# Kernel tuning notes

Hardware: AMD Instinct MI355X
Metric: run time of the kernel (lower is better)

Reference implementation:

```python
import jax, jax.numpy as jnp
import numpy as np

E, L, M, F, S, P = 4, 10, 512, 128, 1000, 10  # envs, labels, max_sample, features, sample_size, batch_len


def setup_inputs() -> dict:
    key = jax.random.key(0)
    k1, k2, k3 = jax.random.split(key, 3)
    data_len = jax.random.randint(k1, (E, L), M // 2, M + 1, dtype=jnp.int32)
    matrix = jax.random.normal(k2, (E, L, M, F), dtype=jnp.float32)
    # zero out padded samples beyond data_len (as shape_to_matrix does)
    pad_mask = jnp.arange(M)[None, None, :, None] < data_len[:, :, None, None]
    matrix = matrix * pad_mask
    params = jnp.eye(F, dtype=jnp.float32) + 0.01 * jax.random.normal(k3, (F, F), dtype=jnp.float32)
    is_train_env = jnp.array([True, True, False, False])
    return {"matrix": matrix, "params": params, "data_len": data_len, "is_train_env": is_train_env}


def reference(matrix, params, data_len, is_train_env):
    lenf = data_len.astype(matrix.dtype)  # [E,L], torch keeps this as float32
    # __init__ preprocessing: normalize by mean std over sample dim (detached in torch)
    std = jax.lax.stop_gradient(jnp.std(matrix, axis=2).mean())
    mat = matrix / std
    # Silverman-style bandwidth on the normalized matrix (detached in torch)
    bw = jax.lax.stop_gradient(1.06 * (M ** (-1.0 / 5.0)) * jnp.std(mat, axis=2).mean())
    offset = jnp.exp(-0.5 / bw ** 2)
    proj = jnp.einsum('elmf,fg->elmg', mat, params)  # [E,L,M,F]
    left = jax.lax.stop_gradient(proj.min())   # .item() in torch -> constant
    right = jax.lax.stop_gradient(proj.max())
    delta = (right - left) / S
    x_grid = jnp.linspace(left, right, S)
    divisor = jnp.sqrt(2.0 * jnp.pi) * bw

    def step(acc, points):  # points: [P] grid chunk
        d2 = (proj[..., None] - points) ** 2                     # [E,L,M,F,P]
        s = jnp.sum(offset ** d2, axis=2)                        # [E,L,F,P]
        # remove contribution of zero-padded samples, then normalize by true count
        corr = (M - lenf)[:, :, None] * (offset ** (points ** 2))[None, None, :]  # [E,L,P]
        r = (s - corr[:, :, None, :]) / lenf[:, :, None, None]   # [E,L,F,P]
        d = jnp.sum(jnp.abs(r[:, None] - r[None, :]), axis=-1)   # [E,E,L,F] pairwise L1 over grid chunk
        return acc + d, None

    store_dis, _ = jax.lax.scan(step, jnp.zeros((E, E, L, F), proj.dtype), x_grid.reshape(S // P, P))
    store_dis = store_dis / divisor  # [E,E,L,F]

    idx = jnp.arange(E)
    upper = idx[:, None] < idx[None, :]                                   # all env pairs i<j
    train_pair = upper & is_train_env[:, None] & is_train_env[None, :]    # train env pairs i<j
    half = store_dis * (delta / 2.0)
    neg = jnp.array(-jnp.inf, half.dtype)
    test_results = jnp.where(upper[:, :, None, None], half, neg).max(axis=(0, 1))        # [L,F]
    train_results = jnp.where(train_pair[:, :, None, None], half, neg).max(axis=(0, 1))  # [L,F]
    train_dis = train_results.max(axis=0).mean()
    test_dis = test_results.max(axis=0).mean()
    return train_results, test_results, train_dis, test_dis
```

## Files before the change

### kernel.cpp

```cpp
#include <hip/hip_runtime.h>
#include <cmath>

#define E_ 4
#define L_ 10
#define M_ 512
#define F_ 128
#define S_ 1000

typedef unsigned int u32;
typedef _Float16 f16;
typedef __attribute__((ext_vector_type(8))) _Float16 v8h;
typedef __attribute__((ext_vector_type(4))) float v4f;

__device__ __forceinline__ float fexp2(float a){
#if __has_builtin(__builtin_amdgcn_exp2f)
  return __builtin_amdgcn_exp2f(a);
#else
  return exp2f(a);
#endif
}


__global__ __launch_bounds__(256) void k_pre(const float* __restrict__ mat,
                       const float* __restrict__ par,
                       float* __restrict__ projT, float* __restrict__ wsf){
  __shared__ float sm[2048];
  int b = blockIdx.x, tid = threadIdx.x;
  if (b >= 1280){
    int el = b - 1280;
    int fq = (tid & 31) * 4, part = tid >> 5;
    const float* base = mat + ((size_t)el * M_ + part*64) * F_;
    float4 s  = make_float4(0.f,0.f,0.f,0.f);
    float4 s2 = make_float4(0.f,0.f,0.f,0.f);
    #pragma unroll 8
    for (int i = 0; i < 64; i++){
      float4 v = *(const float4*)&base[i*F_ + fq];
      s.x += v.x; s.y += v.y; s.z += v.z; s.w += v.w;
      s2.x += v.x*v.x; s2.y += v.y*v.y; s2.z += v.z*v.z; s2.w += v.w*v.w;
    }
    ((float4*)sm)[tid]       = s;
    ((float4*)sm)[256 + tid] = s2;
    __syncthreads();
    for (int g = 4; g >= 1; g >>= 1){
      if (part < g){
        float4 o  = ((float4*)sm)[tid + g*32];
        float4 o2 = ((float4*)sm)[256 + tid + g*32];
        s.x += o.x; s.y += o.y; s.z += o.z; s.w += o.w;
        s2.x += o2.x; s2.y += o2.y; s2.z += o2.z; s2.w += o2.w;
        ((float4*)sm)[tid] = s;
        ((float4*)sm)[256 + tid] = s2;
      }
      __syncthreads();
    }
    if (part == 0){
      *(float4*)&wsf[2576 + el*128 + fq] = s;
      *(float4*)&wsf[7696 + el*128 + fq] = s2;
    }
    return;
  }
  int el = b >> 5, mt = (b & 31) * 16;
  int lane = tid & 63, wave = tid >> 6;
  int q = (lane >> 4) & 3, m16 = lane & 15;
  const float* arow = mat + ((size_t)el * M_ + mt + m16) * F_;
  v4f acc0 = {0.f,0.f,0.f,0.f}, acc1 = {0.f,0.f,0.f,0.f};
  #pragma unroll
  for (int c = 0; c < 4; c++){
    float4 a0 = *(const float4*)&arow[c*32 + q*8];
    float4 a1 = *(const float4*)&arow[c*32 + q*8 + 4];
    v8h af, b0, b1;
    af[0]=(f16)a0.x; af[1]=(f16)a0.y; af[2]=(f16)a0.z; af[3]=(f16)a0.w;
    af[4]=(f16)a1.x; af[5]=(f16)a1.y; af[6]=(f16)a1.z; af[7]=(f16)a1.w;
    const float* pb = par + (c*32 + q*8)*F_ + wave*32 + m16;
    #pragma unroll
    for (int j = 0; j < 8; j++){
      b0[j] = (f16)pb[j*F_];
      b1[j] = (f16)pb[j*F_ + 16];
    }
    acc0 = __builtin_amdgcn_mfma_f32_16x16x32_f16(af, b0, acc0, 0, 0, 0);
    acc1 = __builtin_amdgcn_mfma_f32_16x16x32_f16(af, b1, acc1, 0, 0, 0);
  }
  *(float4*)(projT + ((size_t)el*F_ + wave*32      + m16)*M_ + mt + q*4)
      = make_float4(acc0[0], acc0[1], acc0[2], acc0[3]);
  *(float4*)(projT + ((size_t)el*F_ + wave*32 + 16 + m16)*M_ + mt + q*4)
      = make_float4(acc1[0], acc1[1], acc1[2], acc1[3]);
  float lmin =  3.4e38f, lmax = -3.4e38f;
  #pragma unroll
  for (int r = 0; r < 4; r++){
    lmin = fminf(lmin, fminf(acc0[r], acc1[r]));
    lmax = fmaxf(lmax, fmaxf(acc0[r], acc1[r]));
  }
  #pragma unroll
  for (int d = 32; d >= 1; d >>= 1){
    lmin = fminf(lmin, __shfl_xor(lmin, d, 64));
    lmax = fmaxf(lmax, __shfl_xor(lmax, d, 64));
  }
  if (lane == 0){ sm[wave] = lmin; sm[8+wave] = lmax; }
  __syncthreads();
  if (tid == 0){
    wsf[16   + b] = fminf(fminf(sm[0], sm[1]), fminf(sm[2], sm[3]));
    wsf[1296 + b] = fmaxf(fmaxf(sm[8], sm[9]), fmaxf(sm[10], sm[11]));
  }
}

__global__ __launch_bounds__(1024) void k_red(float* __restrict__ wsf,
                                              float divisor){
  __shared__ float rmn[1024], rmx[1024], rs[1024];
  int tid = threadIdx.x;
  float mn = 3.4e38f, mx = -3.4e38f, s = 0.f;
  for (int i = tid; i < 1280; i += 1024){
    mn = fminf(mn, wsf[16   + i]);
    mx = fmaxf(mx, wsf[1296 + i]);
  }
  for (int i = tid; i < 5120; i += 1024){
    float a  = wsf[2576 + i];
    float a2 = wsf[7696 + i];
    float mean = a * (1.0f/512.0f);
    float var  = a2 * (1.0f/512.0f) - mean*mean;
    s += sqrtf(fmaxf(var, 0.0f));
  }
  rmn[tid] = mn; rmx[tid] = mx; rs[tid] = s;
  __syncthreads();
  for (int g = 512; g >= 1; g >>= 1){
    if (tid < g){
      rmn[tid] = fminf(rmn[tid], rmn[tid+g]);
      rmx[tid] = fmaxf(rmx[tid], rmx[tid+g]);
      rs[tid] += rs[tid+g];
    }
    __syncthreads();
  }
  if (tid == 0){
    float rstd   = 5120.0f / rs[0];
    float leftS  = rmn[0] * rstd;
    float rightS = rmx[0] * rstd;
    float stepFS = (rightS - leftS) * (1.0f/999.0f);
    float inv2   = 1.0f / (2.0f * stepFS);
    wsf[0] = rstd * inv2;
    wsf[1] = leftS * inv2;
    wsf[2] = stepFS;
    wsf[3] = leftS;
    wsf[8] = ((rightS - leftS) * (1.0f/1000.0f)) * 0.5f / divisor;
  }
}

__global__ __launch_bounds__(256) void k_kde(const float* __restrict__ projT,
                      const int* __restrict__ dlen, const float* __restrict__ wsf,
                      float* __restrict__ dpair, float k2c){
  __shared__ __align__(16) float smem[5976];
  int b = blockIdx.x;
  int l = b >> 7, f = b & 127;
  int tid = threadIdx.x, wave = tid >> 6, lane = tid & 63;
  int e = wave;
  const float4* gp = (const float4*)(projT + (((size_t)e * L_ + l) * F_ + f) * M_);
  float4 g0 = gp[lane], g1 = gp[lane + 64];
  float posScale = wsf[0], posOff = wsf[1], stepFS = wsf[2], leftS = wsf[3];
  float lenE = (float)dlen[e*L_ + l];
  float sh = 2.0f * stepFS;
  {
    float4* hz = (float4*)(smem + 1024 + e*824);
    #pragma unroll
    for (int i = 0; i < 4; i++){
      int idx = lane + i*64;
      if (idx < 206) hz[idx] = make_float4(0.f,0.f,0.f,0.f);
    }
  }
  {
    float* tw = smem + 4320 + e*152;
    #pragma unroll
    for (int i = 0; i < 3; i++){
      int t = lane + i*64;
      if (t < 152){
        float v = 0.f;
        if (t >= 8){
          int pr = (t >> 1) - 4;
          int u  = pr - 34;
          float d = (t & 1) ? (float)(2*u-1) * sh : (float)(2*u) * sh;
          v = (pr < 69) ? fexp2(k2c*d*d) : 0.f;
        }
        tw[t] = v;
      }
    }
  }
  {
    float* cw = smem + 4928 + e*256;
    #pragma unroll
    for (int i = 0; i < 4; i++){
      int t = lane + i*64;
      float xc = fmaf((float)(t - 1), 4.0f*stepFS, leftS);
      cw[t] = fexp2(k2c * xc * xc);
    }
  }
  {
    float* hf = smem + 1024 + e*824;
    float pv[8] = {g0.x,g0.y,g0.z,g0.w,g1.x,g1.y,g1.z,g1.w};
    #pragma unroll
    for (int i = 0; i < 8; i++){
      float pos = fmaf(pv[i], posScale, -posOff);
      float n = floorf(pos + 0.5f);
      float d = pos - n;
      float wm = 0.5f*(0.5f-d)*(0.5f-d);
      float wp = 0.5f*(0.5f+d)*(0.5f+d);
      float w0 = 0.75f - d*d;
      int b0 = (int)n + 71;
      int b1 = b0 + 1, b2 = b0 + 2;
      int W0 = b0 + ((b0>>3)<<1);
      int W1 = b1 + ((b1>>3)<<1);
      int W2 = b2 + ((b2>>3)<<1);
      atomicAdd(&hf[W0], wm);
      atomicAdd(&hf[W1], w0);
      atomicAdd(&hf[W2], wp);
    }
  }
  asm volatile("s_waitcnt lgkmcnt(0)");
  __builtin_amdgcn_sched_barrier(0);
  float rlen = 1.0f / lenE;
  float padc = 512.0f - lenE;
  {
    const float2* sK2 = (const float2*)(smem + 4320 + e*152);
    const float* hl = smem + 1024 + e*824 + 10*lane;
    float2 c0 = sK2[72], c1 = sK2[73], c2 = sK2[74], c3 = sK2[75];
    float a0=0.f, a1=0.f, a2=0.f, a3=0.f;
    #pragma unroll
    for (int g = 0; g < 9; g++){
      float2 Hb[8];
      #pragma unroll
      for (int j = 0; j < 8; j++){
        int i = g*8 + j + 1;
        Hb[j] = *(const float2*)&hl[2*i + 2*(i>>2)];
      }
      __builtin_amdgcn_sched_group_barrier(0x100, 8, 0);
      #pragma unroll
      for (int j = 0; j < 8; j++){
        int i = g*8 + j + 1;
        a0 = fmaf(Hb[j].x, c0.x, fmaf(Hb[j].y, c0.y, a0));
        a1 = fmaf(Hb[j].x, c1.x, fmaf(Hb[j].y, c1.y, a1));
        a2 = fmaf(Hb[j].x, c2.x, fmaf(Hb[j].y, c2.y, a2));
        a3 = fmaf(Hb[j].x, c3.x, fmaf(Hb[j].y, c3.y, a3));
        c3 = c2; c2 = c1; c1 = c0; c0 = sK2[72 - i];
      }
    }
    int o0 = 4*lane;
    float4 cr = *(const float4*)&smem[4928 + e*256 + o0];
    float4 stv = make_float4((a0 - padc*cr.x)*rlen, (a1 - padc*cr.y)*rlen,
                             (a2 - padc*cr.z)*rlen, (a3 - padc*cr.w)*rlen);
    *(float4*)&smem[e*256 + o0] = stv;
  }
  __syncthreads();
  float ps[6] = {0,0,0,0,0,0};
  if (tid < 250){
    float x[4][4];
    #pragma unroll
    for (int ee=0; ee<4; ee++){
      const float* st = &smem[ee*256 + tid];
      x[ee][0]=st[0]; x[ee][1]=st[1]; x[ee][2]=st[2]; x[ee][3]=st[3];
    }
    __builtin_amdgcn_sched_group_barrier(0x100, 16, 0);
    #pragma unroll
    for (int k=0; k<4; k++){
      float u = (float)k * 0.25f;
      float um1 = u - 1.0f, um2 = u - 2.0f, up1 = u + 1.0f;
      float w0 = -u * um1 * um2 * (1.0f/6.0f);
      float w1 = up1 * um1 * um2 * 0.5f;
      float w2 = -u * up1 * um2 * 0.5f;
      float w3 = u * up1 * um1 * (1.0f/6.0f);
      float rr[4];
      #pragma unroll
      for (int ee=0; ee<4; ee++)
        rr[ee] = w0*x[ee][0] + w1*x[ee][1] + w2*x[ee][2] + w3*x[ee][3];
      ps[0] += fabsf(rr[0]-rr[1]);
      ps[1] += fabsf(rr[0]-rr[2]);
      ps[2] += fabsf(rr[0]-rr[3]);
      ps[3] += fabsf(rr[1]-rr[2]);
      ps[4] += fabsf(rr[1]-rr[3]);
      ps[5] += fabsf(rr[2]-rr[3]);
    }
  }
  #pragma unroll
  for (int pr=0; pr<6; pr++){
    float v = ps[pr];
    #pragma unroll
    for (int d=32; d>=1; d>>=1) v += __shfl_xor(v, d, 64);
    if (lane == 0) smem[5952 + wave*6 + pr] = v;
  }
  __syncthreads();
  if (tid < 6)
    dpair[tid*1280 + b] = smem[5952+tid] + smem[5958+tid] + smem[5964+tid] + smem[5970+tid];
}

__global__ void k_fin(const float* __restrict__ dpair, const float* __restrict__ wsf,
                      const int* __restrict__ istrain, float* __restrict__ out){
  __shared__ float str[1280], ste[1280];
  __shared__ float s1[128], s2[128];
  int tid = threadIdx.x;
  float hscale = wsf[8];
  bool t0 = istrain[0]!=0, t1 = istrain[1]!=0, t2 = istrain[2]!=0, t3 = istrain[3]!=0;
  bool trn[6] = { t0&&t1, t0&&t2, t0&&t3, t1&&t2, t1&&t3, t2&&t3 };
  for (int idx = tid; idx < 1280; idx += 256){
    float tmax = -INFINITY, trmax = -INFINITY;
    #pragma unroll
    for (int pr=0;pr<6;pr++){
      float h = dpair[pr*1280 + idx] * hscale;
      tmax = fmaxf(tmax, h);
      if (trn[pr]) trmax = fmaxf(trmax, h);
    }
    out[idx]        = trmax;
    out[1280 + idx] = tmax;
    str[idx] = trmax; ste[idx] = tmax;
  }
  __syncthreads();
  if (tid < 128){
    float m1 = -INFINITY, m2 = -INFINITY;
    for (int l=0;l<L_;l++){
      m1 = fmaxf(m1, str[l*F_ + tid]);
      m2 = fmaxf(m2, ste[l*F_ + tid]);
    }
    s1[tid] = m1; s2[tid] = m2;
  }
  __syncthreads();
  for (int g=64; g>=1; g>>=1){
    if (tid < g){ s1[tid] += s1[tid+g]; s2[tid] += s2[tid+g]; }
    __syncthreads();
  }
  if (tid == 0){
    out[2560] = s1[0] * (1.0f/128.0f);
    out[2561] = s2[0] * (1.0f/128.0f);
  }
}

extern "C" void kernel_launch(void* const* d_in, const int* in_sizes, int n_in,
                              void* d_out, int out_size, void* d_ws, size_t ws_size,
                              hipStream_t stream){
  const float* mat = (const float*)d_in[0];
  const float* par = (const float*)d_in[1];
  const int*  dlen = (const int*)d_in[2];
  const int*  istr = (const int*)d_in[3];
  float* out   = (float*)d_out;
  float* wsf   = (float*)d_ws;
  float* dpair = wsf + 12816;
  float* projT = wsf + 20496;

  double bw_d   = 1.06 * pow(512.0, -0.2);
  float  bw     = (float)bw_d;
  float  offset = expf(-0.5f / (bw*bw));
  float  k2c    = (float)(log((double)offset) * 1.4426950408889634);
  float  divisor = sqrtf(6.283185307179586f) * bw;

  k_pre <<<1320, 256, 0, stream>>>(mat, par, projT, wsf);
  k_red <<<1,   1024, 0, stream>>>(wsf, divisor);
  k_kde <<<1280, 256, 0, stream>>>(projT, dlen, wsf, dpair, k2c);
  k_fin <<<1,    256, 0, stream>>>(dpair, wsf, istr, out);
}
```

Baseline: 141.4 us.

## Split per-wave LDS histogram by lane parity to cut atomic contention

Each wave's scatter histogram is split into two copies chosen by lane parity, and the two are summed when read in the convolution loop. The aim is to reduce LDS atomicAdd collisions between neighbouring lanes that hit the same bins. The kernel-weight table is now one copy shared by all waves. Every wave writes the same values into it, which is a benign race. The padding-correction weights are now computed in registers with exp2 instead of being stored in and read from an LDS table. In exchange, LDS use grows, the zeroing pass is larger, and the convolution issues twice as many LDS reads plus extra adds.

```diff
diff --git a/kernel.cpp b/kernel.cpp
--- a/kernel.cpp
+++ b/kernel.cpp
@@ -145,7 +145,7 @@
 __global__ __launch_bounds__(256) void k_kde(const float* __restrict__ projT,
                       const int* __restrict__ dlen, const float* __restrict__ wsf,
                       float* __restrict__ dpair, float k2c){
-  __shared__ __align__(16) float smem[5976];
+  __shared__ __align__(16) float smem[7792];
   int b = blockIdx.x;
   int l = b >> 7, f = b & 127;
   int tid = threadIdx.x, wave = tid >> 6, lane = tid & 63;
@@ -156,15 +156,15 @@
   float lenE = (float)dlen[e*L_ + l];
   float sh = 2.0f * stepFS;
   {
-    float4* hz = (float4*)(smem + 1024 + e*824);
-    #pragma unroll
-    for (int i = 0; i < 4; i++){
+    float4* hz = (float4*)(smem + 1024 + e*1648);
+    #pragma unroll
+    for (int i = 0; i < 7; i++){
       int idx = lane + i*64;
-      if (idx < 206) hz[idx] = make_float4(0.f,0.f,0.f,0.f);
+      if (idx < 412) hz[idx] = make_float4(0.f,0.f,0.f,0.f);
     }
   }
   {
-    float* tw = smem + 4320 + e*152;
+    float* tw = smem + 7616;
     #pragma unroll
     for (int i = 0; i < 3; i++){
       int t = lane + i*64;
@@ -181,16 +181,7 @@
     }
   }
   {
-    float* cw = smem + 4928 + e*256;
-    #pragma unroll
-    for (int i = 0; i < 4; i++){
-      int t = lane + i*64;
-      float xc = fmaf((float)(t - 1), 4.0f*stepFS, leftS);
-      cw[t] = fexp2(k2c * xc * xc);
-    }
-  }
-  {
-    float* hf = smem + 1024 + e*824;
+    float* hf = smem + 1024 + e*1648 + (lane & 1)*824;
     float pv[8] = {g0.x,g0.y,g0.z,g0.w,g1.x,g1.y,g1.z,g1.w};
     #pragma unroll
     for (int i = 0; i < 8; i++){
@@ -215,33 +206,44 @@
   float rlen = 1.0f / lenE;
   float padc = 512.0f - lenE;
   {
-    const float2* sK2 = (const float2*)(smem + 4320 + e*152);
-    const float* hl = smem + 1024 + e*824 + 10*lane;
+    const float2* sK2 = (const float2*)(smem + 7616);
+    const float* hl = smem + 1024 + e*1648 + 10*lane;
     float2 c0 = sK2[72], c1 = sK2[73], c2 = sK2[74], c3 = sK2[75];
     float a0=0.f, a1=0.f, a2=0.f, a3=0.f;
     #pragma unroll
     for (int g = 0; g < 9; g++){
-      float2 Hb[8];
+      float2 HA[8], HB[8];
       #pragma unroll
       for (int j = 0; j < 8; j++){
         int i = g*8 + j + 1;
-        Hb[j] = *(const float2*)&hl[2*i + 2*(i>>2)];
+        int off = 2*i + 2*(i>>2);
+        HA[j] = *(const float2*)&hl[off];
+        HB[j] = *(const float2*)&hl[off + 824];
       }
-      __builtin_amdgcn_sched_group_barrier(0x100, 8, 0);
+      __builtin_amdgcn_sched_group_barrier(0x100, 16, 0);
       #pragma unroll
       for (int j = 0; j < 8; j++){
         int i = g*8 + j + 1;
-        a0 = fmaf(Hb[j].x, c0.x, fmaf(Hb[j].y, c0.y, a0));
-        a1 = fmaf(Hb[j].x, c1.x, fmaf(Hb[j].y, c1.y, a1));
-        a2 = fmaf(Hb[j].x, c2.x, fmaf(Hb[j].y, c2.y, a2));
-        a3 = fmaf(Hb[j].x, c3.x, fmaf(Hb[j].y, c3.y, a3));
+        float hx = HA[j].x + HB[j].x;
+        float hy = HA[j].y + HB[j].y;
+        a0 = fmaf(hx, c0.x, fmaf(hy, c0.y, a0));
+        a1 = fmaf(hx, c1.x, fmaf(hy, c1.y, a1));
+        a2 = fmaf(hx, c2.x, fmaf(hy, c2.y, a2));
+        a3 = fmaf(hx, c3.x, fmaf(hy, c3.y, a3));
         c3 = c2; c2 = c1; c1 = c0; c0 = sK2[72 - i];
       }
     }
     int o0 = 4*lane;
-    float4 cr = *(const float4*)&smem[4928 + e*256 + o0];
-    float4 stv = make_float4((a0 - padc*cr.x)*rlen, (a1 - padc*cr.y)*rlen,
-                             (a2 - padc*cr.z)*rlen, (a3 - padc*cr.w)*rlen);
+    float xc0 = fmaf((float)(o0 - 1), 4.0f*stepFS, leftS);
+    float xc1 = fmaf((float)(o0    ), 4.0f*stepFS, leftS);
+    float xc2 = fmaf((float)(o0 + 1), 4.0f*stepFS, leftS);
+    float xc3 = fmaf((float)(o0 + 2), 4.0f*stepFS, leftS);
+    float cr0 = fexp2(k2c * xc0 * xc0);
+    float cr1 = fexp2(k2c * xc1 * xc1);
+    float cr2 = fexp2(k2c * xc2 * xc2);
+    float cr3 = fexp2(k2c * xc3 * xc3);
+    float4 stv = make_float4((a0 - padc*cr0)*rlen, (a1 - padc*cr1)*rlen,
+                             (a2 - padc*cr2)*rlen, (a3 - padc*cr3)*rlen);
     *(float4*)&smem[e*256 + o0] = stv;
   }
   __syncthreads();
@@ -279,11 +281,11 @@
     float v = ps[pr];
     #pragma unroll
     for (int d=32; d>=1; d>>=1) v += __shfl_xor(v, d, 64);
-    if (lane == 0) smem[5952 + wave*6 + pr] = v;
+    if (lane == 0) smem[7768 + wave*6 + pr] = v;
   }
   __syncthreads();
   if (tid < 6)
-    dpair[tid*1280 + b] = smem[5952+tid] + smem[5958+tid] + smem[5964+tid] + smem[5970+tid];
+    dpair[tid*1280 + b] = smem[7768+tid] + smem[7774+tid] + smem[7780+tid] + smem[7786+tid];
 }
 
 __global__ void k_fin(const float* __restrict__ dpair, const float* __restrict__ wsf,
```

Result: no change. 143.7 us (+1.6%).
